# Optimization experiments

Measured on AMD Instinct MI355X. Metric: run time of the kernel, lower is better.

## Reference

```python
import jax, jax.numpy as jnp
import numpy as np


def _bilinear(x, oh, ow, align_corners):
    # x: [N, C, H, W] -> [N, C, oh, ow], matching torch bilinear semantics
    n, c, h, w = x.shape
    if align_corners:
        ys = jnp.linspace(0.0, h - 1.0, oh)
        xs = jnp.linspace(0.0, w - 1.0, ow)
    else:
        ys = jnp.clip((jnp.arange(oh) + 0.5) * (h / oh) - 0.5, 0.0, h - 1.0)
        xs = jnp.clip((jnp.arange(ow) + 0.5) * (w / ow) - 0.5, 0.0, w - 1.0)
    y0 = jnp.floor(ys).astype(jnp.int32)
    y1 = jnp.minimum(y0 + 1, h - 1)
    x0 = jnp.floor(xs).astype(jnp.int32)
    x1 = jnp.minimum(x0 + 1, w - 1)
    wy = (ys - y0).astype(x.dtype)[None, None, :, None]
    wx = (xs - x0).astype(x.dtype)[None, None, None, :]
    rows = x[:, :, y0, :] * (1.0 - wy) + x[:, :, y1, :] * wy  # [N,C,oh,W]
    out = rows[:, :, :, x0] * (1.0 - wx) + rows[:, :, :, x1] * wx  # [N,C,oh,ow]
    return out


def _minmax_norm(m):
    # per-sample min-max normalize over (C,H,W)
    mn = m.min(axis=(1, 2, 3), keepdims=True)
    mx = m.max(axis=(1, 2, 3), keepdims=True)
    return (m - mn) / (mx - mn)


def setup_inputs() -> dict:
    key = jax.random.key(0)
    k1, k2, k3, k4, k5, k6 = jax.random.split(key, 6)
    B, C, H, W = 32, 256, 56, 56
    Ce, He, We = 128, 28, 28
    return {
        "main_inputs": jax.random.normal(k1, (B, C, H, W), dtype=jnp.float32),
        "embedding_inputs": jax.random.normal(k2, (B, Ce, He, We), dtype=jnp.float32),
        "inference_x": jax.random.uniform(k3, (B, 1, 112, 112), dtype=jnp.float32),
        "conv_w": jax.random.normal(k4, (C, Ce), dtype=jnp.float32) * 0.05,
        "conv_b": jax.random.normal(k5, (C,), dtype=jnp.float32) * 0.05,
        "weight": jax.random.normal(k6, (1,), dtype=jnp.float32),
    }


def reference(main_inputs, embedding_inputs, inference_x, conv_w, conv_b, weight):
    H, W = main_inputs.shape[2], main_inputs.shape[3]
    # interface: bilinear upsample (align_corners=False) + 1x1 conv
    emb = _bilinear(embedding_inputs, H, W, align_corners=False)
    emb = jnp.einsum('nchw,oc->nohw', emb, conv_w) + conv_b[None, :, None, None]
    # channel mean -> per-sample min-max normalize
    mask = _minmax_norm(emb.mean(axis=1, keepdims=True))  # [B,1,H,W]
    # inference mask: bilinear (align_corners=True) to mask resolution
    inf = _bilinear(inference_x, H, W, align_corners=True)
    mask = _minmax_norm(mask * inf)
    a = jax.nn.sigmoid(main_inputs)
    return a * mask * weight[0] + a
```

## Files before the change

kernel.cpp:

```cpp
#include <hip/hip_runtime.h>
#include <math.h>


#define HW_E   784
#define HW_O   3136
#define CE     128
#define CO     256
#define NBATCH 32
#define KSPLIT 4

#define ERED_OFF 256
#define S_OFF    (256 + KSPLIT * NBATCH * HW_E)

__global__ void k_wbar(const float* __restrict__ W, const float* __restrict__ b,
                       float* __restrict__ ws) {
    __shared__ float sb[256];
    int t = threadIdx.x;
    if (t < CE) {
        float acc = 0.f;
        #pragma unroll 8
        for (int o = 0; o < CO; ++o) acc += W[o * CE + t];
        ws[t] = acc * (1.0f / (float)CO);
    }
    sb[t] = b[t];
    __syncthreads();
    for (int s = 128; s > 0; s >>= 1) {
        if (t < s) sb[t] += sb[t + s];
        __syncthreads();
    }
    if (t == 0) ws[128] = sb[0] * (1.0f / (float)CO);
}

__global__ void k_ered(const float* __restrict__ emb, const float* __restrict__ ws,
                       float* __restrict__ ered) {
    __shared__ float swb[CE];
    int t = threadIdx.x;
    if (t < CE) swb[t] = ws[t];
    __syncthreads();
    int gid = blockIdx.x * 256 + t;
    if (gid >= KSPLIT * NBATCH * HW_E) return;
    int out  = gid % (NBATCH * HW_E);
    int part = gid / (NBATCH * HW_E);
    int n = out / HW_E;
    int p = out % HW_E;
    const float* base = emb + (size_t)n * CE * HW_E + (size_t)(part * (CE / KSPLIT)) * HW_E + p;
    const float* wb   = swb + part * (CE / KSPLIT);
    float acc = 0.f;
    #pragma unroll 8
    for (int c = 0; c < CE / KSPLIT; ++c) acc += base[c * HW_E] * wb[c];
    ered[gid] = acc;
}

__device__ inline void block_minmax(float lmin, float lmax, float* red, int t,
                                    float& mn, float& mx) {
    __syncthreads();
    #pragma unroll
    for (int off = 32; off > 0; off >>= 1) {
        lmin = fminf(lmin, __shfl_down(lmin, off, 64));
        lmax = fmaxf(lmax, __shfl_down(lmax, off, 64));
    }
    int wave = t >> 6;
    if ((t & 63) == 0) { red[wave] = lmin; red[4 + wave] = lmax; }
    __syncthreads();
    if (t == 0) {
        red[0] = fminf(fminf(red[0], red[1]), fminf(red[2], red[3]));
        red[4] = fmaxf(fmaxf(red[4], red[5]), fmaxf(red[6], red[7]));
    }
    __syncthreads();
    mn = red[0];
    mx = red[4];
}

__global__ void k_mask(const float* __restrict__ infx, const float* __restrict__ ws,
                       const float* __restrict__ wscalar, float* __restrict__ sout) {
    __shared__ float sE[HW_E];
    __shared__ float sM[HW_O];
    __shared__ float red[8];
    const int n = blockIdx.x;
    const int t = threadIdx.x;
    const float bbar = ws[128];

    for (int p = t; p < HW_E; p += 256) {
        float v = 0.f;
        #pragma unroll
        for (int k = 0; k < KSPLIT; ++k)
            v += ws[ERED_OFF + k * (NBATCH * HW_E) + n * HW_E + p];
        sE[p] = v;
    }
    __syncthreads();

    float lmin = 1e30f, lmax = -1e30f;
    for (int p = t; p < HW_O; p += 256) {
        int oh = p / 56, ow = p % 56;
        float ys = fminf(fmaxf(0.5f * oh - 0.25f, 0.f), 27.f);
        float xs = fminf(fmaxf(0.5f * ow - 0.25f, 0.f), 27.f);
        int y0 = (int)ys, x0 = (int)xs;
        int y1 = min(y0 + 1, 27), x1 = min(x0 + 1, 27);
        float wy = ys - (float)y0, wx = xs - (float)x0;
        float v00 = sE[y0 * 28 + x0], v01 = sE[y0 * 28 + x1];
        float v10 = sE[y1 * 28 + x0], v11 = sE[y1 * 28 + x1];
        float r0 = v00 * (1.f - wy) + v10 * wy;
        float r1 = v01 * (1.f - wy) + v11 * wy;
        float m  = r0 * (1.f - wx) + r1 * wx + bbar;
        sM[p] = m;
        lmin = fminf(lmin, m);
        lmax = fmaxf(lmax, m);
    }
    float mn1, mx1;
    block_minmax(lmin, lmax, red, t, mn1, mx1);
    float inv1 = 1.f / (mx1 - mn1);

    const float step = 111.0f / 55.0f;
    const float* xin = infx + (size_t)n * 112 * 112;
    float lmin2 = 1e30f, lmax2 = -1e30f;
    for (int p = t; p < HW_O; p += 256) {
        int oh = p / 56, ow = p % 56;
        float ys = step * (float)oh, xs = step * (float)ow;
        int y0 = (int)ys, x0 = (int)xs;
        int y1 = min(y0 + 1, 111), x1 = min(x0 + 1, 111);
        float wy = ys - (float)y0, wx = xs - (float)x0;
        float v00 = xin[y0 * 112 + x0], v01 = xin[y0 * 112 + x1];
        float v10 = xin[y1 * 112 + x0], v11 = xin[y1 * 112 + x1];
        float r0 = v00 * (1.f - wy) + v10 * wy;
        float r1 = v01 * (1.f - wy) + v11 * wy;
        float inf = r0 * (1.f - wx) + r1 * wx;
        float p2 = (sM[p] - mn1) * inv1 * inf;
        sM[p] = p2;
        lmin2 = fminf(lmin2, p2);
        lmax2 = fmaxf(lmax2, p2);
    }
    float mn2, mx2;
    block_minmax(lmin2, lmax2, red, t, mn2, mx2);
    float inv2 = 1.f / (mx2 - mn2);
    float wgt = wscalar[0];

    for (int p = t; p < HW_O; p += 256)
        sout[n * HW_O + p] = (sM[p] - mn2) * inv2 * wgt + 1.0f;
}

__global__ void k_main(const float* __restrict__ x, const float* __restrict__ s,
                       float* __restrict__ out, int total4) {
    int stride = gridDim.x * blockDim.x;
    for (int i = blockIdx.x * blockDim.x + threadIdx.x; i < total4; i += stride) {
        float4 v = ((const float4*)x)[i];
        int elem = i * 4;
        int hw = elem % HW_O;
        int n  = elem / (HW_O * CO);
        float4 sv = ((const float4*)s)[(n * HW_O + hw) >> 2];
        float4 o;
        o.x = sv.x / (1.f + expf(-v.x));
        o.y = sv.y / (1.f + expf(-v.y));
        o.z = sv.z / (1.f + expf(-v.z));
        o.w = sv.w / (1.f + expf(-v.w));
        ((float4*)out)[i] = o;
    }
}

extern "C" void kernel_launch(void* const* d_in, const int* in_sizes, int n_in,
                              void* d_out, int out_size, void* d_ws, size_t ws_size,
                              hipStream_t stream) {
    const float* main_in = (const float*)d_in[0];
    const float* emb_in  = (const float*)d_in[1];
    const float* inf_in  = (const float*)d_in[2];
    const float* conv_w  = (const float*)d_in[3];
    const float* conv_b  = (const float*)d_in[4];
    const float* weight  = (const float*)d_in[5];
    float* out = (float*)d_out;
    float* ws  = (float*)d_ws;

    k_wbar<<<1, 256, 0, stream>>>(conv_w, conv_b, ws);

    int nered = KSPLIT * NBATCH * HW_E;
    k_ered<<<(nered + 255) / 256, 256, 0, stream>>>(emb_in, ws, ws + ERED_OFF);

    k_mask<<<NBATCH, 256, 0, stream>>>(inf_in, ws, weight, ws + S_OFF);

    int total4 = out_size / 4;
    k_main<<<2048, 256, 0, stream>>>(main_in, ws + S_OFF, out, total4);
}
```

Before: 231.5 us.

## Fold weight averaging into reduction kernel, drop bias, widen mask block, nontemporal main

Removes the separate single-block weight-mean kernel by having each reduction block compute its own slice of the averaged conv weights. It drops the bias term, since a constant shift cancels in min-max normalization, and doubles the channel split to 8 parts. The mask kernel now runs 1024 threads per batch. The main elementwise kernel drops its grid-stride loop, has each thread handle four float4 vectors with nontemporal loads and stores, and launches a grid sized to cover the whole output. This saves a launch and cuts serial latency, at the cost of redundant weight reads in every reduction block.

```diff
diff --git a/kernel.cpp b/kernel.cpp
--- a/kernel.cpp
+++ b/kernel.cpp
@@ -2,95 +2,95 @@
 #include <math.h>
 
 
-#define HW_E   784
-#define HW_O   3136
-#define CE     128
-#define CO     256
-#define NBATCH 32
-#define KSPLIT 4
+#define HW_E 784
+#define HW_O 3136
+#define CE   128
+#define CO   256
+#define NB   32
+#define KS   8
+#define CPP  (CE / KS)
+#define NPE  (NB * HW_E)
 
-#define ERED_OFF 256
-#define S_OFF    (256 + KSPLIT * NBATCH * HW_E)
+#define ERED_OFF 0
+#define S_OFF    (KS * NPE)
 
-__global__ void k_wbar(const float* __restrict__ W, const float* __restrict__ b,
-                       float* __restrict__ ws) {
-    __shared__ float sb[256];
-    int t = threadIdx.x;
-    if (t < CE) {
-        float acc = 0.f;
-        #pragma unroll 8
-        for (int o = 0; o < CO; ++o) acc += W[o * CE + t];
-        ws[t] = acc * (1.0f / (float)CO);
+typedef float f4 __attribute__((ext_vector_type(4)));
+
+__global__ __launch_bounds__(256) void k_ered(const float* __restrict__ emb,
+                                              const float* __restrict__ W,
+                                              float* __restrict__ ered) {
+    __shared__ float swp[4][CPP];
+    __shared__ float swb[CPP];
+    const int t   = threadIdx.x;
+    const int gid = blockIdx.x * 256 + t;
+    const int part = gid / NPE;
+    const int cb   = part * CPP;
+
+    {
+        const int j  = t & 15;
+        const int oc = t >> 4;
+        const float* wp = W + (size_t)(oc * 16) * CE + cb + j;
+        float a = 0.f;
+        #pragma unroll
+        for (int k = 0; k < 16; ++k) a += wp[(size_t)k * CE];
+        a += __shfl_xor(a, 16, 64);
+        a += __shfl_xor(a, 32, 64);
+        if ((t & 63) < CPP) swp[t >> 6][j] = a;
     }
-    sb[t] = b[t];
     __syncthreads();
-    for (int s = 128; s > 0; s >>= 1) {
-        if (t < s) sb[t] += sb[t + s];
-        __syncthreads();
-    }
-    if (t == 0) ws[128] = sb[0] * (1.0f / (float)CO);
-}
+    if (t < CPP) swb[t] = swp[0][t] + swp[1][t] + swp[2][t] + swp[3][t];
+    __syncthreads();
 
-__global__ void k_ered(const float* __restrict__ emb, const float* __restrict__ ws,
-                       float* __restrict__ ered) {
-    __shared__ float swb[CE];
-    int t = threadIdx.x;
-    if (t < CE) swb[t] = ws[t];
-    __syncthreads();
-    int gid = blockIdx.x * 256 + t;
-    if (gid >= KSPLIT * NBATCH * HW_E) return;
-    int out  = gid % (NBATCH * HW_E);
-    int part = gid / (NBATCH * HW_E);
-    int n = out / HW_E;
-    int p = out % HW_E;
-    const float* base = emb + (size_t)n * CE * HW_E + (size_t)(part * (CE / KSPLIT)) * HW_E + p;
-    const float* wb   = swb + part * (CE / KSPLIT);
+    const int local = gid - part * NPE;
+    const int n = local / HW_E;
+    const int p = local - n * HW_E;
+    const float* base = emb + ((size_t)n * CE + cb) * HW_E + p;
     float acc = 0.f;
-    #pragma unroll 8
-    for (int c = 0; c < CE / KSPLIT; ++c) acc += base[c * HW_E] * wb[c];
+    #pragma unroll
+    for (int c = 0; c < CPP; ++c) acc += base[(size_t)c * HW_E] * swb[c];
     ered[gid] = acc;
 }
 
-__device__ inline void block_minmax(float lmin, float lmax, float* red, int t,
-                                    float& mn, float& mx) {
+__device__ inline void bmm(float lmin, float lmax, float* red, int t,
+                           float& mn, float& mx) {
     __syncthreads();
     #pragma unroll
-    for (int off = 32; off > 0; off >>= 1) {
+    for (int off = 32; off; off >>= 1) {
         lmin = fminf(lmin, __shfl_down(lmin, off, 64));
         lmax = fmaxf(lmax, __shfl_down(lmax, off, 64));
     }
-    int wave = t >> 6;
-    if ((t & 63) == 0) { red[wave] = lmin; red[4 + wave] = lmax; }
+    if ((t & 63) == 0) { red[t >> 6] = lmin; red[16 + (t >> 6)] = lmax; }
     __syncthreads();
     if (t == 0) {
-        red[0] = fminf(fminf(red[0], red[1]), fminf(red[2], red[3]));
-        red[4] = fmaxf(fmaxf(red[4], red[5]), fmaxf(red[6], red[7]));
+        float a = red[0], b = red[16];
+        #pragma unroll
+        for (int i = 1; i < 16; ++i) { a = fminf(a, red[i]); b = fmaxf(b, red[16 + i]); }
+        red[0] = a; red[16] = b;
     }
     __syncthreads();
-    mn = red[0];
-    mx = red[4];
+    mn = red[0]; mx = red[16];
 }
 
-__global__ void k_mask(const float* __restrict__ infx, const float* __restrict__ ws,
-                       const float* __restrict__ wscalar, float* __restrict__ sout) {
+__global__ __launch_bounds__(1024) void k_mask(const float* __restrict__ infx,
+                                               const float* __restrict__ ered,
+                                               const float* __restrict__ wscalar,
+                                               float* __restrict__ sout) {
     __shared__ float sE[HW_E];
     __shared__ float sM[HW_O];
-    __shared__ float red[8];
+    __shared__ float red[32];
     const int n = blockIdx.x;
     const int t = threadIdx.x;
-    const float bbar = ws[128];
 
-    for (int p = t; p < HW_E; p += 256) {
+    if (t < HW_E) {
         float v = 0.f;
         #pragma unroll
-        for (int k = 0; k < KSPLIT; ++k)
-            v += ws[ERED_OFF + k * (NBATCH * HW_E) + n * HW_E + p];
-        sE[p] = v;
+        for (int k = 0; k < KS; ++k) v += ered[k * NPE + n * HW_E + t];
+        sE[t] = v;
     }
     __syncthreads();
 
     float lmin = 1e30f, lmax = -1e30f;
-    for (int p = t; p < HW_O; p += 256) {
+    for (int p = t; p < HW_O; p += 1024) {
         int oh = p / 56, ow = p % 56;
         float ys = fminf(fmaxf(0.5f * oh - 0.25f, 0.f), 27.f);
         float xs = fminf(fmaxf(0.5f * ow - 0.25f, 0.f), 27.f);
@@ -101,19 +101,18 @@
         float v10 = sE[y1 * 28 + x0], v11 = sE[y1 * 28 + x1];
         float r0 = v00 * (1.f - wy) + v10 * wy;
         float r1 = v01 * (1.f - wy) + v11 * wy;
-        float m  = r0 * (1.f - wx) + r1 * wx + bbar;
+        float m  = r0 * (1.f - wx) + r1 * wx;
         sM[p] = m;
-        lmin = fminf(lmin, m);
-        lmax = fmaxf(lmax, m);
+        lmin = fminf(lmin, m); lmax = fmaxf(lmax, m);
     }
     float mn1, mx1;
-    block_minmax(lmin, lmax, red, t, mn1, mx1);
+    bmm(lmin, lmax, red, t, mn1, mx1);
     float inv1 = 1.f / (mx1 - mn1);
 
     const float step = 111.0f / 55.0f;
     const float* xin = infx + (size_t)n * 112 * 112;
     float lmin2 = 1e30f, lmax2 = -1e30f;
-    for (int p = t; p < HW_O; p += 256) {
+    for (int p = t; p < HW_O; p += 1024) {
         int oh = p / 56, ow = p % 56;
         float ys = step * (float)oh, xs = step * (float)ow;
         int y0 = (int)ys, x0 = (int)xs;
@@ -126,34 +125,47 @@
         float inf = r0 * (1.f - wx) + r1 * wx;
         float p2 = (sM[p] - mn1) * inv1 * inf;
         sM[p] = p2;
-        lmin2 = fminf(lmin2, p2);
-        lmax2 = fmaxf(lmax2, p2);
+        lmin2 = fminf(lmin2, p2); lmax2 = fmaxf(lmax2, p2);
     }
     float mn2, mx2;
-    block_minmax(lmin2, lmax2, red, t, mn2, mx2);
+    bmm(lmin2, lmax2, red, t, mn2, mx2);
     float inv2 = 1.f / (mx2 - mn2);
     float wgt = wscalar[0];
 
-    for (int p = t; p < HW_O; p += 256)
+    for (int p = t; p < HW_O; p += 1024)
         sout[n * HW_O + p] = (sM[p] - mn2) * inv2 * wgt + 1.0f;
 }
 
-__global__ void k_main(const float* __restrict__ x, const float* __restrict__ s,
-                       float* __restrict__ out, int total4) {
-    int stride = gridDim.x * blockDim.x;
-    for (int i = blockIdx.x * blockDim.x + threadIdx.x; i < total4; i += stride) {
-        float4 v = ((const float4*)x)[i];
-        int elem = i * 4;
-        int hw = elem % HW_O;
-        int n  = elem / (HW_O * CO);
-        float4 sv = ((const float4*)s)[(n * HW_O + hw) >> 2];
-        float4 o;
-        o.x = sv.x / (1.f + expf(-v.x));
-        o.y = sv.y / (1.f + expf(-v.y));
-        o.z = sv.z / (1.f + expf(-v.z));
-        o.w = sv.w / (1.f + expf(-v.w));
-        ((float4*)out)[i] = o;
-    }
+__global__ __launch_bounds__(256) void k_main(const float* __restrict__ x,
+                                              const float* __restrict__ s,
+                                              float* __restrict__ out, int total4) {
+    const f4* x4 = (const f4*)x;
+    const f4* s4 = (const f4*)s;
+    f4* o4 = (f4*)out;
+    const int q0 = blockIdx.x * 1024 + threadIdx.x;
+
+    int q[4] = { q0, q0 + 256, q0 + 512, q0 + 768 };
+    f4 v[4], sv[4];
+    #pragma unroll
+    for (int j = 0; j < 4; ++j)
+        if (q[j] < total4) v[j] = __builtin_nontemporal_load(&x4[q[j]]);
+    #pragma unroll
+    for (int j = 0; j < 4; ++j)
+        if (q[j] < total4) {
+            int hwq = q[j] % (HW_O / 4);
+            int n   = q[j] / ((HW_O / 4) * CO);
+            sv[j] = s4[n * (HW_O / 4) + hwq];
+        }
+    #pragma unroll
+    for (int j = 0; j < 4; ++j)
+        if (q[j] < total4) {
+            f4 r;
+            r.x = sv[j].x / (1.f + expf(-v[j].x));
+            r.y = sv[j].y / (1.f + expf(-v[j].y));
+            r.z = sv[j].z / (1.f + expf(-v[j].z));
+            r.w = sv[j].w / (1.f + expf(-v[j].w));
+            __builtin_nontemporal_store(r, &o4[q[j]]);
+        }
 }
 
 extern "C" void kernel_launch(void* const* d_in, const int* in_sizes, int n_in,
@@ -163,18 +175,14 @@
     const float* emb_in  = (const float*)d_in[1];
     const float* inf_in  = (const float*)d_in[2];
     const float* conv_w  = (const float*)d_in[3];
-    const float* conv_b  = (const float*)d_in[4];
     const float* weight  = (const float*)d_in[5];
     float* out = (float*)d_out;
     float* ws  = (float*)d_ws;
 
-    k_wbar<<<1, 256, 0, stream>>>(conv_w, conv_b, ws);
-
-    int nered = KSPLIT * NBATCH * HW_E;
-    k_ered<<<(nered + 255) / 256, 256, 0, stream>>>(emb_in, ws, ws + ERED_OFF);
-
-    k_mask<<<NBATCH, 256, 0, stream>>>(inf_in, ws, weight, ws + S_OFF);
+    k_ered<<<KS * NPE / 256, 256, 0, stream>>>(emb_in, conv_w, ws + ERED_OFF);
+    k_mask<<<NB, 1024, 0, stream>>>(inf_in, ws + ERED_OFF, weight, ws + S_OFF);
 
     int total4 = out_size / 4;
-    k_main<<<2048, 256, 0, stream>>>(main_in, ws + S_OFF, out, total4);
+    int blocks = (total4 + 1023) / 1024;
+    k_main<<<blocks, 256, 0, stream>>>(main_in, ws + S_OFF, out, total4);
 }
```

Measured after the change: 205.2 us. -11.4%, faster.
